# Kernel optimization log

Hardware: AMD Instinct MI355X
Metric: run time of the kernel (lower is better)

The kernel has to match this reference:

```python
import jax, jax.numpy as jnp
import numpy as np

NEG = 9e15

def adj_helper(adj):
    n = adj.shape[0]
    a = adj + jnp.eye(n, dtype=adj.dtype)
    d1 = jnp.sqrt(a.sum(axis=-1))[:, None]
    d2 = jnp.sqrt(a.sum(axis=0))[None, :]
    return a / d1 / d2

def gcn(adj, x, Ws):
    a = adj_helper(adj)
    z = x
    for W in Ws:
        z = jax.nn.elu(a @ (z @ W))
    return z

def sage(adj, x, layers):
    deg = jnp.clip(adj.sum(axis=-1, keepdims=True), 1e-5, None)
    a = adj / deg
    z = x
    for (Wp, b, W) in layers:
        h = jax.nn.elu(z @ Wp + b)
        h = a @ h
        z = jax.nn.elu(jnp.concatenate([z, h], axis=1) @ W)
    return z

def sim_graph_cos(h, k):
    n = h.shape[0]
    length = jnp.sqrt(jnp.sum(h * h, axis=-1))          # [n]
    sim = (h @ h.T) / (length[:, None] * length[None, :])
    sim = sim - jnp.eye(n, dtype=sim.dtype) * NEG        # mask self
    val, ids = jax.lax.top_k(sim, k)                     # [n,k]
    rows = jnp.arange(n)[:, None]
    return jnp.zeros_like(sim).at[rows, ids].set(val)

def setup_inputs() -> dict:
    key = jax.random.key(0)
    ks = jax.random.split(key, 16)
    N, F, H, E, K = 6144, 128, 128, 16384, 32
    s = 0.05
    adj = (jax.random.uniform(ks[0], (N, N)) < 0.002).astype(jnp.float32)
    x = jax.random.normal(ks[1], (N, F), dtype=jnp.float32)
    src = jax.random.randint(ks[2], (E,), 0, N)
    dst = jax.random.randint(ks[3], (E,), 0, N)
    labels = (jax.random.uniform(ks[4], (E,)) < 0.5).astype(jnp.float32)
    return {
        "src": src, "dst": dst, "labels": labels, "adj": adj, "x": x,
        "Wg1": jax.random.normal(ks[5], (F, H)) * s,
        "Wg2": jax.random.normal(ks[6], (H, H)) * s,
        "Wp1": jax.random.normal(ks[7], (F, H)) * s,
        "b1": jax.random.normal(ks[8], (1, H)) * s,
        "Ws1": jax.random.normal(ks[9], (F + H, H)) * s,
        "Wp2": jax.random.normal(ks[10], (H, H)) * s,
        "b2": jax.random.normal(ks[11], (1, H)) * s,
        "Ws2": jax.random.normal(ks[12], (H + H, H)) * s,
        "PredW": jax.random.normal(ks[13], (2 * H, 2 * H)) * s,
        "PredB": jax.random.normal(ks[14], (1, 1)) * s,
        "top_k": 32,
    }

def reference(src, dst, labels, adj, x, Wg1, Wg2, Wp1, b1, Ws1, Wp2, b2, Ws2, PredW, PredB, top_k):
    h1 = gcn(adj, x, [Wg1, Wg2])                 # [N,H]
    sim_adj = sim_graph_cos(x, top_k)            # [N,N] top-k sparse (dense-stored)
    h2 = sage(sim_adj, x, [(Wp1, b1, Ws1), (Wp2, b2, Ws2)])  # [N,H]
    h = jnp.concatenate([h1, h2], axis=1)        # [N,2H]
    src_h = h[src]                               # [E,2H]
    dst_h = h[dst]                               # [E,2H]
    logits = jnp.einsum('ed,df,ef->e', src_h, PredW, dst_h) + PredB[0, 0]
    # BCEWithLogitsLoss (mean, numerically stable)
    loss = jnp.mean(jnp.maximum(logits, 0) - logits * labels
                    + jnp.log1p(jnp.exp(-jnp.abs(logits))))
    return loss, logits
```

## Files before the change

### kernel.cpp

```cpp
#include <hip/hip_runtime.h>
#include <hip/hip_bf16.h>
#include <stdint.h>

#define N_NODES 6144
#define FDIM    128
#define EEDGES  16384
#define KTOP    32
#define KSEL    48
#define MAXNBR  64
#define MAXCAND 512
#define NTILES  96
#define GRIDY   16
#define TPB     (NTILES/GRIDY)

typedef short bf16x8 __attribute__((ext_vector_type(8)));
typedef float f32x4  __attribute__((ext_vector_type(4)));

__device__ __forceinline__ float elu_f(float x){ return x > 0.f ? x : expm1f(x); }

__device__ __forceinline__ unsigned short f2bf(float f){
  unsigned int u = __float_as_uint(f);
  u += 0x7FFFu + ((u >> 16) & 1u);
  return (unsigned short)(u >> 16);
}
__device__ __forceinline__ float bf2f(unsigned short h){
  return __uint_as_float(((unsigned int)h) << 16);
}

__global__ __launch_bounds__(256) void adj_scan(const float* __restrict__ adj,
    int* __restrict__ nbr, int* __restrict__ nbrcnt, int* __restrict__ colcnt){
  const int i = blockIdx.x, t = threadIdx.x;
  __shared__ int s_cnt;
  if (t == 0) s_cnt = 0;
  __syncthreads();
  const float4* row = (const float4*)(adj + (size_t)i * N_NODES);
  for (int v = t; v < N_NODES/4; v += 256){
    float4 f = row[v];
    int b = v * 4;
    if (f.x != 0.f){ int s = atomicAdd(&s_cnt,1); if (s < MAXNBR) nbr[i*MAXNBR+s] = b;   atomicAdd(&colcnt[b],1); }
    if (f.y != 0.f){ int s = atomicAdd(&s_cnt,1); if (s < MAXNBR) nbr[i*MAXNBR+s] = b+1; atomicAdd(&colcnt[b+1],1); }
    if (f.z != 0.f){ int s = atomicAdd(&s_cnt,1); if (s < MAXNBR) nbr[i*MAXNBR+s] = b+2; atomicAdd(&colcnt[b+2],1); }
    if (f.w != 0.f){ int s = atomicAdd(&s_cnt,1); if (s < MAXNBR) nbr[i*MAXNBR+s] = b+3; atomicAdd(&colcnt[b+3],1); }
  }
  __syncthreads();
  if (t == 0) nbrcnt[i] = min(s_cnt, MAXNBR);
}

__global__ __launch_bounds__(128) void xprep(const float* __restrict__ x,
    unsigned short* __restrict__ xbf, float* __restrict__ xninv,
    float* __restrict__ cat1){
  const int i = blockIdx.x, t = threadIdx.x;
  float v = x[(size_t)i*FDIM + t];
  xbf[(size_t)i*FDIM + t] = f2bf(v);
  cat1[(size_t)i*256 + t] = v;
  float s = v * v;
  for (int o = 32; o > 0; o >>= 1) s += __shfl_down(s, o, 64);
  __shared__ float ws[2];
  if ((t & 63) == 0) ws[t >> 6] = s;
  __syncthreads();
  if (t == 0) xninv[i] = rsqrtf(ws[0] + ws[1]);
}

__global__ __launch_bounds__(256) void simgemm(const unsigned short* __restrict__ xbf,
    const float* __restrict__ xninv, unsigned short* __restrict__ sim,
    float* __restrict__ gmax){
  const int t    = threadIdx.x;
  const int R0   = blockIdx.x * 32;
  const int tb0  = blockIdx.y * TPB;
  const int lane = t & 63, w = t >> 6;
  const int lr   = lane & 15, q8 = (lane >> 4) * 8, quad = lane >> 4;

  __shared__ unsigned short Abf[32][136];
  __shared__ unsigned short Bbf[64][136];
  __shared__ unsigned short Stile[32][72];
  __shared__ float nrow[32];
  __shared__ float ncol[64];
  __shared__ float wmax[4][32];

  for (int e = t; e < 32*16; e += 256){
    int r = e >> 4, c8 = e & 15;
    *(uint4*)&Abf[r][c8*8] = ((const uint4*)(xbf + (size_t)(R0 + r)*FDIM))[c8];
  }
  if (t < 32) nrow[t] = xninv[R0 + t];

  for (int tb = tb0; tb < tb0 + TPB; ++tb){
    __syncthreads();
    for (int e = t; e < 64*16; e += 256){
      int r = e >> 4, c8 = e & 15;
      *(uint4*)&Bbf[r][c8*8] = ((const uint4*)(xbf + (size_t)(tb*64 + r)*FDIM))[c8];
    }
    if (t < 64) ncol[t] = xninv[tb*64 + t];
    __syncthreads();

    f32x4 acc[2] = {};
#pragma unroll
    for (int kb = 0; kb < 4; ++kb){
      bf16x8 bcol  = *(const bf16x8*)&Bbf[w*16 + lr][kb*32 + q8];
      bf16x8 arow0 = *(const bf16x8*)&Abf[lr      ][kb*32 + q8];
      bf16x8 arow1 = *(const bf16x8*)&Abf[16 + lr ][kb*32 + q8];
      acc[0] = __builtin_amdgcn_mfma_f32_16x16x32_bf16(bcol, arow0, acc[0], 0, 0, 0);
      acc[1] = __builtin_amdgcn_mfma_f32_16x16x32_bf16(bcol, arow1, acc[1], 0, 0, 0);
    }
    const int scol0 = w*16 + quad*4;
    const float nc0 = ncol[scol0], nc1 = ncol[scol0+1],
                nc2 = ncol[scol0+2], nc3 = ncol[scol0+3];
#pragma unroll
    for (int f = 0; f < 2; ++f){
      const int srow = f*16 + lr;
      const float nr = nrow[srow];
      const int grow = R0 + srow, gcol0 = tb*64 + scol0;
      float v0 = acc[f][0]*nr*nc0, v1 = acc[f][1]*nr*nc1,
            v2 = acc[f][2]*nr*nc2, v3 = acc[f][3]*nr*nc3;
      if (grow == gcol0    ) v0 = -2.0f;
      if (grow == gcol0 + 1) v1 = -2.0f;
      if (grow == gcol0 + 2) v2 = -2.0f;
      if (grow == gcol0 + 3) v3 = -2.0f;
      unsigned int h0 = f2bf(v0), h1 = f2bf(v1), h2 = f2bf(v2), h3 = f2bf(v3);
      uint2 p; p.x = h0 | (h1 << 16); p.y = h2 | (h3 << 16);
      *(uint2*)&Stile[srow][scol0] = p;
      float rmax = fmaxf(fmaxf(bf2f(h0), bf2f(h1)), fmaxf(bf2f(h2), bf2f(h3)));
      rmax = fmaxf(rmax, __shfl_xor(rmax, 16, 64));
      rmax = fmaxf(rmax, __shfl_xor(rmax, 32, 64));
      if (quad == 0) wmax[w][srow] = rmax;
    }
    __syncthreads();
    {
      int r = t >> 3, c8 = t & 7;
      *(uint4*)&sim[(size_t)(R0 + r)*N_NODES + tb*64 + c8*8] = *(uint4*)&Stile[r][c8*8];
    }
    if (t < 32){
      float g = fmaxf(fmaxf(wmax[0][t], wmax[1][t]), fmaxf(wmax[2][t], wmax[3][t]));
      gmax[(size_t)(R0 + t)*NTILES + tb] = g;
    }
  }
}

__global__ __launch_bounds__(256) void taukern(const float* __restrict__ gmax,
    float* __restrict__ tau, const int* __restrict__ nbrcnt,
    const int* __restrict__ colcnt, float* __restrict__ d1inv,
    float* __restrict__ d2inv){
  const int R0 = blockIdx.x * 32, t = threadIdx.x;
  {
    int i = blockIdx.x*256 + t;
    if (i < N_NODES){
      d1inv[i] = rsqrtf((float)(nbrcnt[i] + 1));
      d2inv[i] = rsqrtf((float)(colcnt[i] + 1));
    }
  }
  __shared__ float tm[32][97];
  for (int e = t; e < 32*NTILES; e += 256){
    int r = e / NTILES, j = e % NTILES;
    tm[r][j] = gmax[(size_t)(R0 + r)*NTILES + j];
  }
  __syncthreads();
  if (t < 32){
    float m = 0.f;
    for (int k = 0; k < KSEL; ++k){
      m = -3.4e38f; int am = 0;
      for (int j = 0; j < NTILES; ++j){
        float u = tm[t][j];
        if (u > m){ m = u; am = j; }
      }
      tm[t][am] = -3.4e38f;
    }
    tau[R0 + t] = m;
  }
}

__global__ __launch_bounds__(256) void refine_scan(const float* __restrict__ x,
    const float* __restrict__ xninv, const unsigned short* __restrict__ sim,
    const float* __restrict__ tau, float* __restrict__ tval, int* __restrict__ tidx,
    float* __restrict__ deginv){
  const int i = blockIdx.x, t = threadIdx.x;
  __shared__ float xi[128];
  __shared__ float cv[MAXCAND];
  __shared__ int   ci[MAXCAND];
  __shared__ float sel[KTOP];
  __shared__ int   cnt;
  if (t == 0) cnt = 0;
  if (t < 32) *(float4*)&xi[t*4] = *(const float4*)(x + (size_t)i*FDIM + t*4);
  __syncthreads();
  const float taui = tau[i];
  const uint4* srow = (const uint4*)(sim + (size_t)i*N_NODES);
  for (int v8 = t; v8 < N_NODES/8; v8 += 256){
    uint4 u = srow[v8];
    const unsigned short* h = (const unsigned short*)&u;
#pragma unroll
    for (int q = 0; q < 8; ++q){
      if (bf2f(h[q]) >= taui){
        int s = atomicAdd(&cnt, 1);
        if (s < MAXCAND) ci[s] = v8*8 + q;
      }
    }
  }
  __syncthreads();
  int n = cnt; if (n > MAXCAND) n = MAXCAND;
  const float ni = xninv[i];
  const int part = t & 3, cb = t >> 2;
  for (int c0 = 0; c0 < n; c0 += 64){
    const int c = c0 + cb;
    float acc = 0.f;
    int idx = 0;
    if (c < n){
      idx = ci[c];
      const float* xc = x + (size_t)idx*FDIM + part*32;
#pragma unroll
      for (int q = 0; q < 8; ++q){
        float4 f = *(const float4*)(xc + q*4);
        const float* a = &xi[part*32 + q*4];
        acc += a[0]*f.x + a[1]*f.y + a[2]*f.z + a[3]*f.w;
      }
    }
    acc += __shfl_xor(acc, 1, 64);
    acc += __shfl_xor(acc, 2, 64);
    if (c < n && part == 0) cv[c] = acc * ni * xninv[idx];
  }
  __syncthreads();
  for (int c = t; c < n; c += 256){
    float v = cv[c]; int id = ci[c];
    int rank = 0;
    for (int j = 0; j < n; ++j){
      float u = cv[j];
      if (u > v || (u == v && ci[j] < id)) rank++;
    }
    if (rank < KTOP){
      tval[(size_t)i*KTOP + rank] = v;
      tidx[(size_t)i*KTOP + rank] = id;
      sel[rank] = v;
    }
  }
  __syncthreads();
  if (t == 0){
    float s = 0.f;
    for (int q = 0; q < KTOP; ++q) s += sel[q];
    deginv[i] = 1.0f / fmaxf(s, 1e-5f);
  }
}

template<int M>
__global__ __launch_bounds__(256) void gemm_k(const float* __restrict__ A, int lda,
    const float* __restrict__ B, const float* __restrict__ bias,
    float* __restrict__ C, int ldc, int K, int act){
  const int t = threadIdx.x;
  const int R0 = blockIdx.x * 32, C0 = blockIdx.y * 64;
  const int rg = t >> 4, cg = t & 15;
  __shared__ float Alds[32][34];
  __shared__ float Blds[32][68];
  float4 acc0 = {0,0,0,0}, acc1 = {0,0,0,0};
  for (int kc = 0; kc < K; kc += 32){
    __syncthreads();
    { int r = t >> 3, k0 = (t & 7) * 4;
      float4 f = *(const float4*)(A + (size_t)(R0 + r)*lda + kc + k0);
      Alds[k0+0][r] = f.x; Alds[k0+1][r] = f.y; Alds[k0+2][r] = f.z; Alds[k0+3][r] = f.w; }
#pragma unroll
    for (int e = 0; e < 2; ++e){
      int idx = t + e*256;
      int k = idx >> 4, m4 = idx & 15;
      *(float4*)&Blds[k][m4*4] = *(const float4*)(B + (size_t)(kc + k)*M + C0 + m4*4);
    }
    __syncthreads();
#pragma unroll
    for (int k = 0; k < 32; ++k){
      float2 a = *(const float2*)&Alds[k][rg*2];
      float4 b = *(const float4*)&Blds[k][cg*4];
      acc0.x += a.x*b.x; acc0.y += a.x*b.y; acc0.z += a.x*b.z; acc0.w += a.x*b.w;
      acc1.x += a.y*b.x; acc1.y += a.y*b.y; acc1.z += a.y*b.z; acc1.w += a.y*b.w;
    }
  }
  const int r0 = R0 + rg*2, c0 = C0 + cg*4;
  float4 bb = {0,0,0,0};
  if (bias) bb = *(const float4*)&bias[c0];
  acc0.x += bb.x; acc0.y += bb.y; acc0.z += bb.z; acc0.w += bb.w;
  acc1.x += bb.x; acc1.y += bb.y; acc1.z += bb.z; acc1.w += bb.w;
  if (act){
    acc0.x = elu_f(acc0.x); acc0.y = elu_f(acc0.y); acc0.z = elu_f(acc0.z); acc0.w = elu_f(acc0.w);
    acc1.x = elu_f(acc1.x); acc1.y = elu_f(acc1.y); acc1.z = elu_f(acc1.z); acc1.w = elu_f(acc1.w);
  }
  *(float4*)&C[(size_t)r0*ldc + c0] = acc0;
  *(float4*)&C[(size_t)(r0+1)*ldc + c0] = acc1;
}

__global__ __launch_bounds__(128) void spmm_gcn(const float* __restrict__ T,
    const int* __restrict__ nbr, const int* __restrict__ nbrcnt,
    const float* __restrict__ d1inv, const float* __restrict__ d2inv,
    float* __restrict__ C, int ldc){
  const int i = blockIdx.x, t = threadIdx.x;
  float acc = T[(size_t)i*FDIM + t] * d2inv[i];
  const int cnt = nbrcnt[i];
  const int* nb = nbr + (size_t)i*MAXNBR;
  for (int s = 0; s < cnt; ++s){
    int j = nb[s];
    acc += T[(size_t)j*FDIM + t] * d2inv[j];
  }
  C[(size_t)i*ldc + t] = elu_f(acc * d1inv[i]);
}

__global__ __launch_bounds__(128) void spmm_sage(const float* __restrict__ P,
    const float* __restrict__ tval, const int* __restrict__ tidx,
    const float* __restrict__ deginv, float* __restrict__ C, int ldc){
  const int i = blockIdx.x, t = threadIdx.x;
  float acc = 0.f;
  const float* vv = tval + (size_t)i*KTOP;
  const int*   ii = tidx + (size_t)i*KTOP;
  for (int s = 0; s < KTOP; ++s)
    acc += vv[s] * P[(size_t)ii[s]*FDIM + t];
  C[(size_t)i*ldc + t] = acc * deginv[i];
}

__global__ __launch_bounds__(256) void edge_loss(const int* __restrict__ src,
    const int* __restrict__ dst, const float* __restrict__ labels,
    const float* __restrict__ HP, const float* __restrict__ hcat,
    const float* __restrict__ predB, float* __restrict__ out,
    float* __restrict__ partial){
  const int t = threadIdx.x;
  const int e = blockIdx.x*4 + (t >> 6);
  const int lane = t & 63;
  const int s = src[e], d = dst[e];
  const float* hp = HP   + (size_t)s*256;
  const float* hc = hcat + (size_t)d*256;
  float acc = 0.f;
  for (int k = lane; k < 256; k += 64) acc += hp[k] * hc[k];
  for (int o = 32; o > 0; o >>= 1) acc += __shfl_down(acc, o, 64);
  __shared__ float terms[4];
  if (lane == 0){
    float l = acc + predB[0];
    out[1 + e] = l;
    float y = labels[e];
    terms[t >> 6] = fmaxf(l, 0.f) - l*y + log1pf(expf(-fabsf(l)));
  }
  __syncthreads();
  if (t == 0) partial[blockIdx.x] = terms[0] + terms[1] + terms[2] + terms[3];
}

__global__ __launch_bounds__(256) void reduce_loss(const float* __restrict__ partial,
    float* __restrict__ out){
  const int t = threadIdx.x, lane = t & 63, w = t >> 6;
  float s = 0.f;
  for (int i = t; i < EEDGES/4; i += 256) s += partial[i];
  for (int o = 32; o > 0; o >>= 1) s += __shfl_down(s, o, 64);
  __shared__ float ws[4];
  if (lane == 0) ws[w] = s;
  __syncthreads();
  if (t == 0) out[0] = (ws[0] + ws[1] + ws[2] + ws[3]) * (1.0f / EEDGES);
}

extern "C" void kernel_launch(void* const* d_in, const int* in_sizes, int n_in,
                              void* d_out, int out_size, void* d_ws, size_t ws_size,
                              hipStream_t stream){
  (void)in_sizes; (void)n_in; (void)out_size; (void)ws_size;
  const int*   src    = (const int*)d_in[0];
  const int*   dst    = (const int*)d_in[1];
  const float* labels = (const float*)d_in[2];
  const float* adj    = (const float*)d_in[3];
  const float* x      = (const float*)d_in[4];
  const float* Wg1    = (const float*)d_in[5];
  const float* Wg2    = (const float*)d_in[6];
  const float* Wp1    = (const float*)d_in[7];
  const float* b1     = (const float*)d_in[8];
  const float* Ws1    = (const float*)d_in[9];
  const float* Wp2    = (const float*)d_in[10];
  const float* b2     = (const float*)d_in[11];
  const float* Ws2    = (const float*)d_in[12];
  const float* PredW  = (const float*)d_in[13];
  const float* PredB  = (const float*)d_in[14];

  char* ws = (char*)d_ws;
  size_t off = 0;
  auto alloc = [&](size_t bytes)->void*{
    void* p = ws + off; off += (bytes + 255) & ~(size_t)255; return p; };

  int*   colcnt = (int*)  alloc((size_t)N_NODES*4);
  int*   nbrcnt = (int*)  alloc((size_t)N_NODES*4);
  int*   nbr    = (int*)  alloc((size_t)N_NODES*MAXNBR*4);
  float* d1inv  = (float*)alloc((size_t)N_NODES*4);
  float* d2inv  = (float*)alloc((size_t)N_NODES*4);
  float* xninv  = (float*)alloc((size_t)N_NODES*4);
  unsigned short* xbf = (unsigned short*)alloc((size_t)N_NODES*FDIM*2);
  float* tval   = (float*)alloc((size_t)N_NODES*KTOP*4);
  int*   tidx   = (int*)  alloc((size_t)N_NODES*KTOP*4);
  float* dginv  = (float*)alloc((size_t)N_NODES*4);
  float* gmax   = (float*)alloc((size_t)N_NODES*NTILES*4);
  float* tau    = (float*)alloc((size_t)N_NODES*4);
  float* partial= (float*)alloc((size_t)(EEDGES/4)*4);
  float* T      = (float*)alloc((size_t)N_NODES*FDIM*4);
  float* cat1   = (float*)alloc((size_t)N_NODES*256*4);
  float* cat2   = (float*)alloc((size_t)N_NODES*256*4);
  float* hcat   = (float*)alloc((size_t)N_NODES*256*4);
  unsigned short* sim = (unsigned short*)alloc((size_t)N_NODES*N_NODES*2);
  float* z1     = cat2;
  float* out    = (float*)d_out;

  hipMemsetAsync(colcnt, 0, (size_t)N_NODES*4, stream);

  adj_scan   <<<N_NODES, 256, 0, stream>>>(adj, nbr, nbrcnt, colcnt);
  xprep      <<<N_NODES, 128, 0, stream>>>(x, xbf, xninv, cat1);
  simgemm    <<<dim3(N_NODES/32, GRIDY), 256, 0, stream>>>(xbf, xninv, sim, gmax);
  taukern    <<<N_NODES/32, 256, 0, stream>>>(gmax, tau, nbrcnt, colcnt, d1inv, d2inv);
  refine_scan<<<N_NODES, 256, 0, stream>>>(x, xninv, sim, tau, tval, tidx, dginv);

  gemm_k<128><<<dim3(N_NODES/32, 2), 256, 0, stream>>>(x,  FDIM, Wg1, nullptr, T, FDIM, 128, 0);
  spmm_gcn   <<<N_NODES, 128, 0, stream>>>(T, nbr, nbrcnt, d1inv, d2inv, z1, FDIM);
  gemm_k<128><<<dim3(N_NODES/32, 2), 256, 0, stream>>>(z1, FDIM, Wg2, nullptr, T, FDIM, 128, 0);
  spmm_gcn   <<<N_NODES, 128, 0, stream>>>(T, nbr, nbrcnt, d1inv, d2inv, hcat, 256);

  gemm_k<128><<<dim3(N_NODES/32, 2), 256, 0, stream>>>(x, FDIM, Wp1, b1, T, FDIM, 128, 1);
  spmm_sage  <<<N_NODES, 128, 0, stream>>>(T, tval, tidx, dginv, cat1 + 128, 256);
  gemm_k<128><<<dim3(N_NODES/32, 2), 256, 0, stream>>>(cat1, 256, Ws1, nullptr, cat2, 256, 256, 1);

  gemm_k<128><<<dim3(N_NODES/32, 2), 256, 0, stream>>>(cat2, 256, Wp2, b2, T, FDIM, 128, 1);
  spmm_sage  <<<N_NODES, 128, 0, stream>>>(T, tval, tidx, dginv, cat2 + 128, 256);
  gemm_k<128><<<dim3(N_NODES/32, 2), 256, 0, stream>>>(cat2, 256, Ws2, nullptr, hcat + 128, 256, 256, 1);

  gemm_k<256><<<dim3(N_NODES/32, 4), 256, 0, stream>>>(hcat, 256, PredW, nullptr, cat1, 256, 256, 0);
  edge_loss  <<<EEDGES/4, 256, 0, stream>>>(src, dst, labels, cat1, hcat, PredB, out, partial);
  reduce_loss<<<1, 256, 0, stream>>>(partial, out);
}
```

Baseline: 558.0 us.

## Merge small kernels to cut launches and fold tau selection into refine

Merges adj_scan and xprep into one prep launch. Folds the per-row tau selection into refine_scan using a rank-based parallel selection over tile maxima, and moves the degree-inverse computation into a new dual GEMM. That GEMM computes x@Wg1 and the biased ELU of x@Wp1 together, sharing the A tile. The first GCN and SAGE sparse aggregations now run as one paired launch. The aim is fewer kernel launches and serial gaps, plus a single read of x for two GEMMs, at the cost of heterogeneous blocks within a launch.

```diff
diff --git a/kernel.cpp b/kernel.cpp
--- a/kernel.cpp
+++ b/kernel.cpp
@@ -27,38 +27,40 @@
   return __uint_as_float(((unsigned int)h) << 16);
 }
 
-__global__ __launch_bounds__(256) void adj_scan(const float* __restrict__ adj,
-    int* __restrict__ nbr, int* __restrict__ nbrcnt, int* __restrict__ colcnt){
-  const int i = blockIdx.x, t = threadIdx.x;
-  __shared__ int s_cnt;
-  if (t == 0) s_cnt = 0;
-  __syncthreads();
-  const float4* row = (const float4*)(adj + (size_t)i * N_NODES);
-  for (int v = t; v < N_NODES/4; v += 256){
-    float4 f = row[v];
-    int b = v * 4;
-    if (f.x != 0.f){ int s = atomicAdd(&s_cnt,1); if (s < MAXNBR) nbr[i*MAXNBR+s] = b;   atomicAdd(&colcnt[b],1); }
-    if (f.y != 0.f){ int s = atomicAdd(&s_cnt,1); if (s < MAXNBR) nbr[i*MAXNBR+s] = b+1; atomicAdd(&colcnt[b+1],1); }
-    if (f.z != 0.f){ int s = atomicAdd(&s_cnt,1); if (s < MAXNBR) nbr[i*MAXNBR+s] = b+2; atomicAdd(&colcnt[b+2],1); }
-    if (f.w != 0.f){ int s = atomicAdd(&s_cnt,1); if (s < MAXNBR) nbr[i*MAXNBR+s] = b+3; atomicAdd(&colcnt[b+3],1); }
-  }
-  __syncthreads();
-  if (t == 0) nbrcnt[i] = min(s_cnt, MAXNBR);
-}
-
-__global__ __launch_bounds__(128) void xprep(const float* __restrict__ x,
-    unsigned short* __restrict__ xbf, float* __restrict__ xninv,
-    float* __restrict__ cat1){
-  const int i = blockIdx.x, t = threadIdx.x;
-  float v = x[(size_t)i*FDIM + t];
-  xbf[(size_t)i*FDIM + t] = f2bf(v);
-  cat1[(size_t)i*256 + t] = v;
-  float s = v * v;
-  for (int o = 32; o > 0; o >>= 1) s += __shfl_down(s, o, 64);
-  __shared__ float ws[2];
-  if ((t & 63) == 0) ws[t >> 6] = s;
-  __syncthreads();
-  if (t == 0) xninv[i] = rsqrtf(ws[0] + ws[1]);
+__global__ __launch_bounds__(256) void prep(const float* __restrict__ adj,
+    const float* __restrict__ x, int* __restrict__ nbr, int* __restrict__ nbrcnt,
+    int* __restrict__ colcnt, unsigned short* __restrict__ xbf,
+    float* __restrict__ xninv, float* __restrict__ cat1){
+  const int b = blockIdx.x, t = threadIdx.x;
+  if (b < N_NODES){
+    const int i = b;
+    __shared__ int s_cnt;
+    if (t == 0) s_cnt = 0;
+    __syncthreads();
+    const float4* row = (const float4*)(adj + (size_t)i * N_NODES);
+    for (int v = t; v < N_NODES/4; v += 256){
+      float4 f = row[v];
+      int c = v * 4;
+      if (f.x != 0.f){ int s = atomicAdd(&s_cnt,1); if (s < MAXNBR) nbr[i*MAXNBR+s] = c;   atomicAdd(&colcnt[c],1); }
+      if (f.y != 0.f){ int s = atomicAdd(&s_cnt,1); if (s < MAXNBR) nbr[i*MAXNBR+s] = c+1; atomicAdd(&colcnt[c+1],1); }
+      if (f.z != 0.f){ int s = atomicAdd(&s_cnt,1); if (s < MAXNBR) nbr[i*MAXNBR+s] = c+2; atomicAdd(&colcnt[c+2],1); }
+      if (f.w != 0.f){ int s = atomicAdd(&s_cnt,1); if (s < MAXNBR) nbr[i*MAXNBR+s] = c+3; atomicAdd(&colcnt[c+3],1); }
+    }
+    __syncthreads();
+    if (t == 0) nbrcnt[i] = min(s_cnt, MAXNBR);
+  } else {
+    const int i = (b - N_NODES)*2 + (t >> 7);
+    const int tl = t & 127;
+    float v = x[(size_t)i*FDIM + tl];
+    xbf[(size_t)i*FDIM + tl] = f2bf(v);
+    cat1[(size_t)i*256 + tl] = v;
+    float s = v * v;
+    for (int o = 32; o > 0; o >>= 1) s += __shfl_down(s, o, 64);
+    __shared__ float ws[4];
+    if ((t & 63) == 0) ws[t >> 6] = s;
+    __syncthreads();
+    if (tl == 0) xninv[i] = rsqrtf(ws[(t>>7)*2] + ws[(t>>7)*2 + 1]);
+  }
 }
 
 __global__ __launch_bounds__(256) void simgemm(const unsigned short* __restrict__ xbf,
@@ -135,52 +137,32 @@
   }
 }
 
-__global__ __launch_bounds__(256) void taukern(const float* __restrict__ gmax,
-    float* __restrict__ tau, const int* __restrict__ nbrcnt,
-    const int* __restrict__ colcnt, float* __restrict__ d1inv,
-    float* __restrict__ d2inv){
-  const int R0 = blockIdx.x * 32, t = threadIdx.x;
-  {
-    int i = blockIdx.x*256 + t;
-    if (i < N_NODES){
-      d1inv[i] = rsqrtf((float)(nbrcnt[i] + 1));
-      d2inv[i] = rsqrtf((float)(colcnt[i] + 1));
-    }
-  }
-  __shared__ float tm[32][97];
-  for (int e = t; e < 32*NTILES; e += 256){
-    int r = e / NTILES, j = e % NTILES;
-    tm[r][j] = gmax[(size_t)(R0 + r)*NTILES + j];
-  }
-  __syncthreads();
-  if (t < 32){
-    float m = 0.f;
-    for (int k = 0; k < KSEL; ++k){
-      m = -3.4e38f; int am = 0;
-      for (int j = 0; j < NTILES; ++j){
-        float u = tm[t][j];
-        if (u > m){ m = u; am = j; }
-      }
-      tm[t][am] = -3.4e38f;
-    }
-    tau[R0 + t] = m;
-  }
-}
-
 __global__ __launch_bounds__(256) void refine_scan(const float* __restrict__ x,
     const float* __restrict__ xninv, const unsigned short* __restrict__ sim,
-    const float* __restrict__ tau, float* __restrict__ tval, int* __restrict__ tidx,
+    const float* __restrict__ gmax, float* __restrict__ tval, int* __restrict__ tidx,
     float* __restrict__ deginv){
   const int i = blockIdx.x, t = threadIdx.x;
   __shared__ float xi[128];
+  __shared__ float gm[NTILES];
+  __shared__ float tauv;
   __shared__ float cv[MAXCAND];
   __shared__ int   ci[MAXCAND];
   __shared__ float sel[KTOP];
   __shared__ int   cnt;
   if (t == 0) cnt = 0;
   if (t < 32) *(float4*)&xi[t*4] = *(const float4*)(x + (size_t)i*FDIM + t*4);
-  __syncthreads();
-  const float taui = tau[i];
+  if (t < NTILES) gm[t] = gmax[(size_t)i*NTILES + t];
+  __syncthreads();
+  if (t < NTILES){
+    float v = gm[t]; int rank = 0;
+    for (int j = 0; j < NTILES; ++j){
+      float u = gm[j];
+      if (u > v || (u == v && j < t)) rank++;
+    }
+    if (rank == KSEL-1) tauv = v;
+  }
+  __syncthreads();
+  const float taui = tauv;
   const uint4* srow = (const uint4*)(sim + (size_t)i*N_NODES);
   for (int v8 = t; v8 < N_NODES/8; v8 += 256){
     uint4 u = srow[v8];
@@ -235,6 +217,58 @@
     for (int q = 0; q < KTOP; ++q) s += sel[q];
     deginv[i] = 1.0f / fmaxf(s, 1e-5f);
   }
+}
+
+__global__ __launch_bounds__(256) void gemm_dual(const float* __restrict__ A,
+    const float* __restrict__ B1, const float* __restrict__ B2,
+    const float* __restrict__ bias2, float* __restrict__ C1, float* __restrict__ C2,
+    const int* __restrict__ nbrcnt, const int* __restrict__ colcnt,
+    float* __restrict__ d1inv, float* __restrict__ d2inv){
+  const int t = threadIdx.x;
+  const int R0 = blockIdx.x * 32, C0 = blockIdx.y * 64;
+  if (blockIdx.y == 0 && t < 32){
+    int i = R0 + t;
+    d1inv[i] = rsqrtf((float)(nbrcnt[i] + 1));
+    d2inv[i] = rsqrtf((float)(colcnt[i] + 1));
+  }
+  const int rg = t >> 4, cg = t & 15;
+  __shared__ float Alds[32][34];
+  __shared__ float B1lds[32][68];
+  __shared__ float B2lds[32][68];
+  float4 p0 = {0,0,0,0}, p1 = {0,0,0,0};
+  float4 q0 = {0,0,0,0}, q1 = {0,0,0,0};
+  for (int kc = 0; kc < FDIM; kc += 32){
+    __syncthreads();
+    { int r = t >> 3, k0 = (t & 7) * 4;
+      float4 f = *(const float4*)(A + (size_t)(R0 + r)*FDIM + kc + k0);
+      Alds[k0+0][r] = f.x; Alds[k0+1][r] = f.y; Alds[k0+2][r] = f.z; Alds[k0+3][r] = f.w; }
+#pragma unroll
+    for (int e = 0; e < 2; ++e){
+      int idx = t + e*256;
+      int k = idx >> 4, m4 = idx & 15;
+      *(float4*)&B1lds[k][m4*4] = *(const float4*)(B1 + (size_t)(kc + k)*FDIM + C0 + m4*4);
+      *(float4*)&B2lds[k][m4*4] = *(const float4*)(B2 + (size_t)(kc + k)*FDIM + C0 + m4*4);
+    }
+    __syncthreads();
+#pragma unroll
+    for (int k = 0; k < 32; ++k){
+      float2 a = *(const float2*)&Alds[k][rg*2];
+      float4 b = *(const float4*)&B1lds[k][cg*4];
+      float4 c = *(const float4*)&B2lds[k][cg*4];
+      p0.x += a.x*b.x; p0.y += a.x*b.y; p0.z += a.x*b.z; p0.w += a.x*b.w;
+      p1.x += a.y*b.x; p1.y += a.y*b.y; p1.z += a.y*b.z; p1.w += a.y*b.w;
+      q0.x += a.x*c.x; q0.y += a.x*c.y; q0.z += a.x*c.z; q0.w += a.x*c.w;
+      q1.x += a.y*c.x; q1.y += a.y*c.y; q1.z += a.y*c.z; q1.w += a.y*c.w;
+    }
+  }
+  const int r0 = R0 + rg*2, c0 = C0 + cg*4;
+  *(float4*)&C1[(size_t)r0*FDIM + c0] = p0;
+  *(float4*)&C1[(size_t)(r0+1)*FDIM + c0] = p1;
+  float4 bb = *(const float4*)&bias2[c0];
+  q0.x = elu_f(q0.x + bb.x); q0.y = elu_f(q0.y + bb.y); q0.z = elu_f(q0.z + bb.z); q0.w = elu_f(q0.w + bb.w);
+  q1.x = elu_f(q1.x + bb.x); q1.y = elu_f(q1.y + bb.y); q1.z = elu_f(q1.z + bb.z); q1.w = elu_f(q1.w + bb.w);
+  *(float4*)&C2[(size_t)r0*FDIM + c0] = q0;
+  *(float4*)&C2[(size_t)(r0+1)*FDIM + c0] = q1;
 }
 
 template<int M>
@@ -305,6 +339,35 @@
   for (int s = 0; s < KTOP; ++s)
     acc += vv[s] * P[(size_t)ii[s]*FDIM + t];
   C[(size_t)i*ldc + t] = acc * deginv[i];
+}
+
+__global__ __launch_bounds__(128) void spmm_pair(const float* __restrict__ T1,
+    const int* __restrict__ nbr, const int* __restrict__ nbrcnt,
+    const float* __restrict__ d1inv, const float* __restrict__ d2inv,
+    float* __restrict__ z1,
+    const float* __restrict__ T2, const float* __restrict__ tval,
+    const int* __restrict__ tidx, const float* __restrict__ deginv,
+    float* __restrict__ cat1r){
+  const int b = blockIdx.x, t = threadIdx.x;
+  if (b < N_NODES){
+    const int i = b;
+    float acc = T1[(size_t)i*FDIM + t] * d2inv[i];
+    const int cnt = nbrcnt[i];
+    const int* nb = nbr + (size_t)i*MAXNBR;
+    for (int s = 0; s < cnt; ++s){
+      int j = nb[s];
+      acc += T1[(size_t)j*FDIM + t] * d2inv[j];
+    }
+    z1[(size_t)i*FDIM + t] = elu_f(acc * d1inv[i]);
+  } else {
+    const int i = b - N_NODES;
+    float acc = 0.f;
+    const float* vv = tval + (size_t)i*KTOP;
+    const int*   ii = tidx + (size_t)i*KTOP;
+    for (int s = 0; s < KTOP; ++s)
+      acc += vv[s] * T2[(size_t)ii[s]*FDIM + t];
+    cat1r[(size_t)i*256 + t] = acc * deginv[i];
+  }
 }
 
 __global__ __launch_bounds__(256) void edge_loss(const int* __restrict__ src,
@@ -380,9 +443,9 @@
   int*   tidx   = (int*)  alloc((size_t)N_NODES*KTOP*4);
   float* dginv  = (float*)alloc((size_t)N_NODES*4);
   float* gmax   = (float*)alloc((size_t)N_NODES*NTILES*4);
-  float* tau    = (float*)alloc((size_t)N_NODES*4);
   float* partial= (float*)alloc((size_t)(EEDGES/4)*4);
-  float* T      = (float*)alloc((size_t)N_NODES*FDIM*4);
+  float* T1     = (float*)alloc((size_t)N_NODES*FDIM*4);
+  float* T2     = (float*)alloc((size_t)N_NODES*FDIM*4);
   float* cat1   = (float*)alloc((size_t)N_NODES*256*4);
   float* cat2   = (float*)alloc((size_t)N_NODES*256*4);
   float* hcat   = (float*)alloc((size_t)N_NODES*256*4);
@@ -392,23 +455,22 @@
 
   hipMemsetAsync(colcnt, 0, (size_t)N_NODES*4, stream);
 
-  adj_scan   <<<N_NODES, 256, 0, stream>>>(adj, nbr, nbrcnt, colcnt);
-  xprep      <<<N_NODES, 128, 0, stream>>>(x, xbf, xninv, cat1);
+  prep       <<<N_NODES + N_NODES/2, 256, 0, stream>>>(adj, x, nbr, nbrcnt, colcnt, xbf, xninv, cat1);
   simgemm    <<<dim3(N_NODES/32, GRIDY), 256, 0, stream>>>(xbf, xninv, sim, gmax);
-  taukern    <<<N_NODES/32, 256, 0, stream>>>(gmax, tau, nbrcnt, colcnt, d1inv, d2inv);
-  refine_scan<<<N_NODES, 256, 0, stream>>>(x, xninv, sim, tau, tval, tidx, dginv);
-
-  gemm_k<128><<<dim3(N_NODES/32, 2), 256, 0, stream>>>(x,  FDIM, Wg1, nullptr, T, FDIM, 128, 0);
-  spmm_gcn   <<<N_NODES, 128, 0, stream>>>(T, nbr, nbrcnt, d1inv, d2inv, z1, FDIM);
-  gemm_k<128><<<dim3(N_NODES/32, 2), 256, 0, stream>>>(z1, FDIM, Wg2, nullptr, T, FDIM, 128, 0);
-  spmm_gcn   <<<N_NODES, 128, 0, stream>>>(T, nbr, nbrcnt, d1inv, d2inv, hcat, 256);
-
-  gemm_k<128><<<dim3(N_NODES/32, 2), 256, 0, stream>>>(x, FDIM, Wp1, b1, T, FDIM, 128, 1);
-  spmm_sage  <<<N_NODES, 128, 0, stream>>>(T, tval, tidx, dginv, cat1 + 128, 256);
+  refine_scan<<<N_NODES, 256, 0, stream>>>(x, xninv, sim, gmax, tval, tidx, dginv);
+
+  gemm_dual  <<<dim3(N_NODES/32, 2), 256, 0, stream>>>(x, Wg1, Wp1, b1, T1, T2,
+                                                       nbrcnt, colcnt, d1inv, d2inv);
+  spmm_pair  <<<2*N_NODES, 128, 0, stream>>>(T1, nbr, nbrcnt, d1inv, d2inv, z1,
+                                             T2, tval, tidx, dginv, cat1 + 128);
+
+  gemm_k<128><<<dim3(N_NODES/32, 2), 256, 0, stream>>>(z1, FDIM, Wg2, nullptr, T1, FDIM, 128, 0);
+  spmm_gcn   <<<N_NODES, 128, 0, stream>>>(T1, nbr, nbrcnt, d1inv, d2inv, hcat, 256);
+
   gemm_k<128><<<dim3(N_NODES/32, 2), 256, 0, stream>>>(cat1, 256, Ws1, nullptr, cat2, 256, 256, 1);
 
-  gemm_k<128><<<dim3(N_NODES/32, 2), 256, 0, stream>>>(cat2, 256, Wp2, b2, T, FDIM, 128, 1);
-  spmm_sage  <<<N_NODES, 128, 0, stream>>>(T, tval, tidx, dginv, cat2 + 128, 256);
+  gemm_k<128><<<dim3(N_NODES/32, 2), 256, 0, stream>>>(cat2, 256, Wp2, b2, T1, FDIM, 128, 1);
+  spmm_sage  <<<N_NODES, 128, 0, stream>>>(T1, tval, tidx, dginv, cat2 + 128, 256);
   gemm_k<128><<<dim3(N_NODES/32, 2), 256, 0, stream>>>(cat2, 256, Ws2, nullptr, hcat + 128, 256, 256, 1);
 
   gemm_k<256><<<dim3(N_NODES/32, 4), 256, 0, stream>>>(hcat, 256, PredW, nullptr, cat1, 256, 256, 0);
```

New measurement: 483.8 us. 13.3% less time.
